# Optimization experiments

Measured on AMD Instinct MI355X. Metric: run time of the kernel, lower is better.

## Reference

```python
import jax, jax.numpy as jnp
import numpy as np

B, D_IN, H, D_OUT = 2048, 1024, 2048, 1024
MAX_STEPS = 12
EPS = 0.01


def setup_inputs() -> dict:
    key = jax.random.key(0)
    ks = jax.random.split(key, 8)
    s_in = 1.0 / np.sqrt(D_IN + H)
    s_h = 1.0 / np.sqrt(H)
    return {
        "x": jax.random.normal(ks[0], (B, D_IN), jnp.float32),
        "h": jax.random.normal(ks[1], (B, H), jnp.float32),
        "W_hidden": jax.random.normal(ks[2], (H, D_IN + H), jnp.float32) * s_in,
        "b_hidden": jnp.zeros((H,), jnp.float32),
        "w_halt": jax.random.normal(ks[3], (H,), jnp.float32) * s_h,
        "b_halt": jnp.float32(-2.0),  # bias low so several ponder steps are taken
        "W_out": jax.random.normal(ks[4], (D_OUT, H), jnp.float32) * s_h,
        "b_out": jnp.zeros((D_OUT,), jnp.float32),
    }


def reference(x, h, W_hidden, b_hidden, w_halt, b_halt, W_out, b_out):
    # Batched ACT halting loop, unrolled to MAX_STEPS via lax.scan.
    def step(s, t):
        # step 0 of the original uses x+1 as a "first step" flag
        xin = jnp.where(t == 0, x + 1.0, x)          # [B, D_IN]
        z = jnp.concatenate([xin, s], axis=-1)        # [B, D_IN+H]
        s_new = z @ W_hidden.T + b_hidden             # [B, H]
        p = jax.nn.sigmoid(s_new @ w_halt + b_halt)   # [B]
        out = s_new @ W_out.T + b_out                 # [B, D_OUT]
        return s_new, (s_new, p, out)

    _, (states, probs, outs) = jax.lax.scan(step, h, jnp.arange(MAX_STEPS))
    # states: [T,B,H], probs: [T,B], outs: [T,B,D_OUT]

    cum = jnp.cumsum(probs, axis=0)                   # [T,B]
    reached = cum >= (1.0 - EPS)
    # first step where cumulative halt prob crosses the threshold (cap at T-1)
    n = jnp.where(jnp.any(reached, axis=0), jnp.argmax(reached, axis=0), MAX_STEPS - 1)  # [B]

    t_idx = jnp.arange(MAX_STEPS)[:, None]            # [T,1]
    before = t_idx < n[None, :]                       # [T,B]
    R = 1.0 - jnp.sum(jnp.where(before, probs, 0.0), axis=0)  # [B] remainder
    w = jnp.where(before, probs, jnp.where(t_idx == n[None, :], R[None, :], 0.0))  # [T,B]

    output = jnp.einsum("tb,tbd->bd", w, outs)        # [B, D_OUT]
    hidden = jnp.einsum("tb,tbh->bh", w, states)      # [B, H]
    ponder = (n + 1).astype(jnp.float32) + R          # [B]
    return output, hidden, ponder
```

## Files before the change

kernel.cpp:

```cpp
#include <hip/hip_runtime.h>
#include <hip/hip_bf16.h>
#include <cstdint>

#define B_SZ   2048
#define D_INN  1024
#define H_SZ   2048
#define D_OUTN 1024
#define TMAX   12
#define LDW    3072
#define NSL    12
#define SLC    256

typedef _Float16 f16;
typedef __attribute__((ext_vector_type(8))) _Float16 f16x8;
typedef __attribute__((ext_vector_type(4))) float    f32x4;

typedef const __attribute__((address_space(1))) uint32_t* gptr_t;
typedef __attribute__((address_space(3))) uint32_t*       lptr_t;
__device__ inline void gld16(const void* g, void* l) {
    __builtin_amdgcn_global_load_lds((gptr_t)g, (lptr_t)l, 16, 0, 0);
}

template<int BN>
__global__ __launch_bounds__(512, 4) void gemm16(
    const f16* __restrict__ A, int lda,
    const f16* __restrict__ Bm, int ldb,
    const f16*  __restrict__ Cadd16,
    const float* __restrict__ radd,
    float* __restrict__ Cf,
    f16* __restrict__ Cs,
    int ldc, int K, int nx)
{
    constexpr int WN = BN / 64;
    constexpr int NV = (BN == 128) ? 3 : 2;
    __shared__ __align__(16) f16 As[3][64 * 64];
    __shared__ __align__(16) f16 Bs[3][BN * 64];
    const int tid  = threadIdx.x;
    const int wave = tid >> 6;
    const int lane = tid & 63;

    const int nwg = gridDim.x;
    const int cpx = nwg >> 3;
    const int bid = (blockIdx.x & 7) * cpx + (blockIdx.x >> 3);
    const int m0 = (bid / nx) * 64, n0 = (bid % nx) * BN;

    const int wr = wave >> 2, wc = wave & 3;
    const int fr = lane & 15, fq = lane >> 4;

    const int acs = tid ^ ((tid >> 3) & 7);
    const f16* gA = A + (size_t)(m0 + (acs >> 3)) * lda + (acs & 7) * 8;
    const int adst = wave << 9;
    const int bcs1 = tid ^ ((tid >> 3) & 7);
    const f16* gB1 = Bm + (size_t)(n0 + (bcs1 >> 3)) * ldb + (bcs1 & 7) * 8;
    const int bdst1 = wave << 9;
    const f16* gB2 = nullptr;
    int bdst2 = 0;
    if constexpr (BN == 128) {
        const int bc2 = tid + 512;
        const int bcs2 = bc2 ^ ((bc2 >> 3) & 7);
        gB2 = Bm + (size_t)(n0 + (bcs2 >> 3)) * ldb + (bcs2 & 7) * 8;
        bdst2 = 4096 + (wave << 9);
    }

    int offA[2][2], offB[WN][2];
#pragma unroll
    for (int m = 0; m < 2; ++m)
#pragma unroll
        for (int ks = 0; ks < 2; ++ks) {
            const int row = wr * 32 + m * 16 + fr;
            offA[m][ks] = row * 64 + (((ks * 4 + fq) ^ (row & 7)) << 3);
        }
#pragma unroll
    for (int n = 0; n < WN; ++n)
#pragma unroll
        for (int ks = 0; ks < 2; ++ks) {
            const int row = wc * (WN * 16) + n * 16 + fr;
            offB[n][ks] = row * 64 + (((ks * 4 + fq) ^ (row & 7)) << 3);
        }

    auto STAGE = [&](int buf, int ko) {
        gld16(gA + ko,  &As[buf][0] + adst);
        gld16(gB1 + ko, &Bs[buf][0] + bdst1);
        if constexpr (BN == 128) gld16(gB2 + ko, &Bs[buf][0] + bdst2);
    };

    f32x4 acc[2][WN] = {};

    STAGE(0, 0);
    const int nk = K >> 6;
    int cur = 0;
    for (int ki = 0; ki < nk; ++ki) {
        const int nxt = (cur == 2) ? 0 : cur + 1;
        if (ki + 1 < nk) {
            STAGE(nxt, (ki + 1) << 6);
            asm volatile("s_waitcnt vmcnt(%0)" :: "i"(NV) : "memory");
        } else {
            asm volatile("s_waitcnt vmcnt(0)" ::: "memory");
        }
        __builtin_amdgcn_s_barrier();
        asm volatile("" ::: "memory");

        f16x8 a[2][2], b[WN][2];
#pragma unroll
        for (int m = 0; m < 2; ++m)
#pragma unroll
            for (int ks = 0; ks < 2; ++ks)
                a[m][ks] = *(const f16x8*)(&As[cur][offA[m][ks]]);
#pragma unroll
        for (int n = 0; n < WN; ++n)
#pragma unroll
            for (int ks = 0; ks < 2; ++ks)
                b[n][ks] = *(const f16x8*)(&Bs[cur][offB[n][ks]]);
#pragma unroll
        for (int ks = 0; ks < 2; ++ks)
#pragma unroll
            for (int m = 0; m < 2; ++m)
#pragma unroll
                for (int n = 0; n < WN; ++n)
                    acc[m][n] = __builtin_amdgcn_mfma_f32_16x16x32_f16(
                        a[m][ks], b[n][ks], acc[m][n], 0, 0, 0);
        cur = nxt;
    }

#pragma unroll
    for (int m = 0; m < 2; ++m) {
#pragma unroll
        for (int n = 0; n < WN; ++n) {
#pragma unroll
            for (int r = 0; r < 4; ++r) {
                const int row = m0 + wr * 32 + m * 16 + fq * 4 + r;
                const int col = n0 + wc * (WN * 16) + n * 16 + fr;
                const size_t o = (size_t)row * ldc + col;
                float v = acc[m][n][r];
                if (Cadd16) v += (float)Cadd16[o];
                if (radd)   v += radd[col];
                if (Cf) Cf[o] = v;
                if (Cs) Cs[o] = (f16)v;
            }
        }
    }
}

__global__ __launch_bounds__(256) void hidacc(
    const f16* __restrict__ s0, const f16* __restrict__ s1,
    const f16* __restrict__ s2, const float* __restrict__ Wmat,
    int tbase, float* __restrict__ hidden, f16* __restrict__ hid16)
{
    const int b = blockIdx.x;
    const float w0 = Wmat[(size_t)(tbase + 0) * B_SZ + b];
    const float w1 = Wmat[(size_t)(tbase + 1) * B_SZ + b];
    const float w2 = Wmat[(size_t)(tbase + 2) * B_SZ + b];
    const bool first = (tbase == 0);
    const bool last  = (tbase == TMAX - 3);
    if (!last && w0 == 0.f && w1 == 0.f && w2 == 0.f) return;

    const int tid = threadIdx.x;
    const size_t o = (size_t)b * H_SZ + tid * 8;
    float hv[8];
    if (first) {
#pragma unroll
        for (int j = 0; j < 8; ++j) hv[j] = 0.f;
    } else {
        const float4 h0 = *(const float4*)(hidden + o);
        const float4 h1 = *(const float4*)(hidden + o + 4);
        hv[0]=h0.x; hv[1]=h0.y; hv[2]=h0.z; hv[3]=h0.w;
        hv[4]=h1.x; hv[5]=h1.y; hv[6]=h1.z; hv[7]=h1.w;
    }
    if (w0 != 0.f) {
        const f16x8 v = *(const f16x8*)(s0 + o);
#pragma unroll
        for (int j = 0; j < 8; ++j) hv[j] += w0 * (float)v[j];
    }
    if (w1 != 0.f) {
        const f16x8 v = *(const f16x8*)(s1 + o);
#pragma unroll
        for (int j = 0; j < 8; ++j) hv[j] += w1 * (float)v[j];
    }
    if (w2 != 0.f) {
        const f16x8 v = *(const f16x8*)(s2 + o);
#pragma unroll
        for (int j = 0; j < 8; ++j) hv[j] += w2 * (float)v[j];
    }
    *(float4*)(hidden + o)     = make_float4(hv[0], hv[1], hv[2], hv[3]);
    *(float4*)(hidden + o + 4) = make_float4(hv[4], hv[5], hv[6], hv[7]);
    if (last) {
        f16x8 hh;
#pragma unroll
        for (int j = 0; j < 8; ++j) hh[j] = (f16)hv[j];
        *(f16x8*)(hid16 + o) = hh;
    }
}

__global__ __launch_bounds__(256) void cast16(
    const float* __restrict__ src, int ld, int cols,
    f16* __restrict__ dst, int total8)
{
    const int i = blockIdx.x * 256 + threadIdx.x;
    if (i >= total8) return;
    const int idx = i * 8;
    const int r = idx / cols, c = idx % cols;
    const float4 v0 = *(const float4*)(src + (size_t)r * ld + c);
    const float4 v1 = *(const float4*)(src + (size_t)r * ld + c + 4);
    f16x8 o;
    o[0]=(f16)v0.x; o[1]=(f16)v0.y; o[2]=(f16)v0.z; o[3]=(f16)v0.w;
    o[4]=(f16)v1.x; o[5]=(f16)v1.y; o[6]=(f16)v1.z; o[7]=(f16)v1.w;
    *(f16x8*)(dst + idx) = o;
}

__global__ __launch_bounds__(256) void rowsum_kernel(
    const float* __restrict__ W, int ld, int K, float* __restrict__ out)
{
    const int j = blockIdx.x;
    const int tid = threadIdx.x;
    float s = 0.f;
    for (int k = tid; k < K; k += 256) s += W[(size_t)j * ld + k];
#pragma unroll
    for (int off = 32; off; off >>= 1) s += __shfl_down(s, off);
    __shared__ float red[4];
    if ((tid & 63) == 0) red[tid >> 6] = s;
    __syncthreads();
    if (tid == 0) out[j] = red[0] + red[1] + red[2] + red[3];
}

__global__ __launch_bounds__(256) void transpose_w(
    const float* __restrict__ in, float* __restrict__ out, int R, int C)
{
    __shared__ float t[32][33];
    const int bc = blockIdx.x * 32, br = blockIdx.y * 32;
    const int tx = threadIdx.x & 31, ty = threadIdx.x >> 5;
#pragma unroll
    for (int i = 0; i < 32; i += 8)
        t[ty + i][tx] = in[(size_t)(br + ty + i) * C + bc + tx];
    __syncthreads();
#pragma unroll
    for (int i = 0; i < 32; i += 8)
        out[(size_t)(bc + ty + i) * R + br + tx] = t[tx][ty + i];
}

__global__ __launch_bounds__(256) void init_u0(
    const float* __restrict__ w, double* __restrict__ u)
{
    const int i = blockIdx.x * 256 + threadIdx.x;
    if (i < H_SZ) u[i] = (double)w[i];
}

__global__ __launch_bounds__(256) void gemv_t(
    const float* __restrict__ WT, const double* __restrict__ uin,
    double* __restrict__ uout)
{
    const int i = blockIdx.x;
    const int tid = threadIdx.x;
    const float* row = WT + (size_t)(D_INN + i) * H_SZ;
    double acc = 0.0;
    for (int j = tid; j < H_SZ; j += 256) acc += (double)row[j] * uin[j];
#pragma unroll
    for (int off = 32; off; off >>= 1) acc += __shfl_down(acc, off);
    __shared__ double red[4];
    if ((tid & 63) == 0) red[tid >> 6] = acc;
    __syncthreads();
    if (tid == 0) uout[i] = red[0] + red[1] + red[2] + red[3];
}

__global__ __launch_bounds__(256) void batch_wx(
    const float* __restrict__ WT, const double* __restrict__ U,
    double* __restrict__ XU, double* __restrict__ XS)
{
    const int k = blockIdx.x;
    const int tid = threadIdx.x;
    const float* row = WT + (size_t)k * H_SZ;
    double au[TMAX] = {}, av[TMAX] = {};
    for (int j = tid; j < H_SZ; j += 256) {
        const double w = (double)row[j];
        double pref = 0.0;
#pragma unroll
        for (int t = 0; t < TMAX; ++t) {
            const double u = U[(size_t)t * H_SZ + j];
            pref += u;
            au[t] += w * u;
            av[t] += w * pref;
        }
    }
    __shared__ double red[4][2 * TMAX];
#pragma unroll
    for (int t = 0; t < TMAX; ++t) {
#pragma unroll
        for (int off = 32; off; off >>= 1) {
            au[t] += __shfl_down(au[t], off);
            av[t] += __shfl_down(av[t], off);
        }
    }
    if ((tid & 63) == 0) {
#pragma unroll
        for (int t = 0; t < TMAX; ++t) {
            red[tid >> 6][t] = au[t];
            red[tid >> 6][TMAX + t] = av[t];
        }
    }
    __syncthreads();
    if (tid == 0) {
#pragma unroll
        for (int t = 0; t < TMAX; ++t) {
            XS[(size_t)t * D_INN + k] = red[0][t] + red[1][t] + red[2][t] + red[3][t];
            XU[(size_t)t * D_INN + k] = red[0][TMAX+t] + red[1][TMAX+t]
                                      + red[2][TMAX+t] + red[3][TMAX+t];
        }
    }
}

__global__ __launch_bounds__(256) void e_kernel(
    const double* __restrict__ XS, const double* __restrict__ U,
    const float* __restrict__ bh, double* __restrict__ E)
{
    const int t = blockIdx.x;
    const int tid = threadIdx.x;
    double a = 0.0;
    for (int k = tid; k < D_INN; k += 256) a += XS[(size_t)t * D_INN + k];
    for (int j = tid; j < H_SZ; j += 256) {
        double v = 0.0;
        for (int s = 0; s <= t; ++s) v += U[(size_t)s * H_SZ + j];
        a += v * (double)bh[j];
    }
#pragma unroll
    for (int off = 32; off; off >>= 1) a += __shfl_down(a, off);
    __shared__ double red[4];
    if ((tid & 63) == 0) red[tid >> 6] = a;
    __syncthreads();
    if (tid == 0) E[t] = red[0] + red[1] + red[2] + red[3];
}

__global__ __launch_bounds__(256) void d_part(
    const float* __restrict__ h, const float* __restrict__ x,
    const double* __restrict__ U, const double* __restrict__ XU,
    double* __restrict__ part)
{
    __shared__ double Us[TMAX][SLC];
    const int blk = blockIdx.x;
    const int sl  = blk % NSL;
    const int br  = (blk / NSL) * 32;
    const int tid = threadIdx.x;
    const int col0 = sl * SLC;
    const bool isH = col0 < H_SZ;
#pragma unroll
    for (int t = 0; t < TMAX; ++t)
        Us[t][tid] = isH ? U[(size_t)(t + 1) * H_SZ + col0 + tid]
                         : XU[(size_t)t * D_INN + (col0 - H_SZ) + tid];
    __syncthreads();
    const int lane8 = tid & 7;
    const int row   = tid >> 3;
    const float* src = isH ? (h + (size_t)(br + row) * H_SZ + col0)
                           : (x + (size_t)(br + row) * D_INN + (col0 - H_SZ));
    double acc[TMAX] = {};
#pragma unroll
    for (int i = 0; i < 8; ++i) {
        const int c = i * 32 + lane8 * 4;
        const float4 v4 = *(const float4*)(src + c);
        const float vv[4] = {v4.x, v4.y, v4.z, v4.w};
#pragma unroll
        for (int j = 0; j < 4; ++j) {
            const double v = (double)vv[j];
#pragma unroll
            for (int t = 0; t < TMAX; ++t) acc[t] += v * Us[t][c + j];
        }
    }
#pragma unroll
    for (int t = 0; t < TMAX; ++t) {
        acc[t] += __shfl_xor(acc[t], 1, 64);
        acc[t] += __shfl_xor(acc[t], 2, 64);
        acc[t] += __shfl_xor(acc[t], 4, 64);
    }
    if (lane8 == 0) {
#pragma unroll
        for (int t = 0; t < TMAX; ++t)
            part[((size_t)(br + row) * NSL + sl) * TMAX + t] = acc[t];
    }
}

__global__ __launch_bounds__(256) void sched_kernel(
    const double* __restrict__ part, const double* __restrict__ E,
    const float* __restrict__ b_halt,
    float* __restrict__ Wmat, float* __restrict__ ponder)
{
    const int b = blockIdx.x * 256 + threadIdx.x;
    if (b >= B_SZ) return;
    const float bh = b_halt[0];
    float cum = 0.f, R = 0.f;
    int n = -1;
    float w[TMAX];
#pragma unroll
    for (int t = 0; t < TMAX; ++t) {
        double dd = E[t];
#pragma unroll
        for (int sl = 0; sl < NSL; ++sl)
            dd += part[((size_t)b * NSL + sl) * TMAX + t];
        const float p = 1.f / (1.f + expf(-((float)dd + bh)));
        if (n < 0) {
            const float c = cum + p;
            if (c >= 0.99f || t == TMAX - 1) { n = t; R = 1.f - cum; w[t] = R; }
            else { w[t] = p; cum = c; }
        } else {
            w[t] = 0.f;
        }
    }
    ponder[b] = (float)(n + 1) + R;
#pragma unroll
    for (int t = 0; t < TMAX; ++t) Wmat[(size_t)t * B_SZ + b] = w[t];
}

extern "C" void kernel_launch(void* const* d_in, const int* in_sizes, int n_in,
                              void* d_out, int out_size, void* d_ws, size_t ws_size,
                              hipStream_t stream)
{
    const float* x        = (const float*)d_in[0];
    const float* h        = (const float*)d_in[1];
    const float* W_hidden = (const float*)d_in[2];
    const float* b_hidden = (const float*)d_in[3];
    const float* w_halt   = (const float*)d_in[4];
    const float* b_halt   = (const float*)d_in[5];
    const float* W_out    = (const float*)d_in[6];
    const float* b_out    = (const float*)d_in[7];

    float* out    = (float*)d_out;
    float* output = out;
    float* hidden = out + (size_t)B_SZ * D_OUTN;
    float* ponder = hidden + (size_t)B_SZ * H_SZ;

    double* U    = (double*)d_ws;
    double* XU   = U  + (size_t)(TMAX + 1) * H_SZ;
    double* XS   = XU + (size_t)TMAX * D_INN;
    double* E    = XS + (size_t)TMAX * D_INN;
    double* part = E + 16;
    float* rsum  = (float*)(part + (size_t)B_SZ * NSL * TMAX);
    float* Wmat  = rsum + H_SZ;
    float* WT    = Wmat + (size_t)TMAX * B_SZ;
    f16* xc16  = (f16*)WT;
    f16* S2    = (f16*)(WT + (size_t)2 * 1024 * 1024);
    f16* hid16 = (f16*)(WT + (size_t)4 * 1024 * 1024);
    f16* xh   = (f16*)(WT + (size_t)LDW * H_SZ);
    f16* Wxh  = xh  + (size_t)B_SZ * D_INN;
    f16* S0   = xh;
    f16* h16  = Wxh + (size_t)H_SZ * D_INN;
    f16* S1   = h16 + (size_t)B_SZ * H_SZ;
    f16* Wsh  = S1  + (size_t)B_SZ * H_SZ;
    f16* Woh  = Wsh + (size_t)H_SZ * H_SZ;

    const dim3 blk(256);
    const dim3 gblk(512);

    cast16<<<dim3(B_SZ * D_INN / 8 / 256), blk, 0, stream>>>(
        x, D_INN, D_INN, xh, B_SZ * D_INN / 8);
    cast16<<<dim3(B_SZ * H_SZ / 8 / 256), blk, 0, stream>>>(
        h, H_SZ, H_SZ, h16, B_SZ * H_SZ / 8);
    cast16<<<dim3(H_SZ * D_INN / 8 / 256), blk, 0, stream>>>(
        W_hidden, LDW, D_INN, Wxh, H_SZ * D_INN / 8);
    cast16<<<dim3(H_SZ * H_SZ / 8 / 256), blk, 0, stream>>>(
        W_hidden + D_INN, LDW, H_SZ, Wsh, H_SZ * H_SZ / 8);
    cast16<<<dim3(D_OUTN * H_SZ / 8 / 256), blk, 0, stream>>>(
        W_out, H_SZ, H_SZ, Woh, D_OUTN * H_SZ / 8);

    rowsum_kernel<<<dim3(H_SZ), blk, 0, stream>>>(W_hidden, LDW, D_INN, rsum);

    transpose_w<<<dim3(LDW / 32, H_SZ / 32), blk, 0, stream>>>(
        W_hidden, WT, H_SZ, LDW);
    init_u0<<<dim3(H_SZ / 256), blk, 0, stream>>>(w_halt, U);
    for (int k = 0; k < TMAX; ++k)
        gemv_t<<<dim3(H_SZ), blk, 0, stream>>>(WT, U + (size_t)k * H_SZ,
                                               U + (size_t)(k + 1) * H_SZ);
    batch_wx<<<dim3(D_INN), blk, 0, stream>>>(WT, U, XU, XS);
    e_kernel<<<dim3(TMAX), blk, 0, stream>>>(XS, U, b_hidden, E);
    d_part<<<dim3((B_SZ / 32) * NSL), blk, 0, stream>>>(h, x, U, XU, part);
    sched_kernel<<<dim3(B_SZ / 256), blk, 0, stream>>>(part, E, b_halt,
                                                       Wmat, ponder);

    gemm16<128><<<dim3((B_SZ / 64) * (H_SZ / 128)), gblk, 0, stream>>>(
        xh, D_INN, Wxh, D_INN, nullptr, b_hidden, nullptr, xc16,
        H_SZ, D_INN, H_SZ / 128);

    f16* Sb[3] = {S0, S1, S2};
    const f16* prev = h16;
    for (int t = 0; t < TMAX; ++t) {
        f16* curS = Sb[t % 3];
        gemm16<128><<<dim3((B_SZ / 64) * (H_SZ / 128)), gblk, 0, stream>>>(
            prev, H_SZ, Wsh, H_SZ, xc16, (t == 0) ? rsum : nullptr,
            nullptr, curS, H_SZ, H_SZ, H_SZ / 128);
        prev = curS;
        if ((t % 3) == 2)
            hidacc<<<dim3(B_SZ), blk, 0, stream>>>(
                S0, S1, S2, Wmat, t - 2, hidden, hid16);
    }

    gemm16<64><<<dim3((B_SZ / 64) * (D_OUTN / 64)), gblk, 0, stream>>>(
        hid16, H_SZ, Woh, H_SZ, nullptr, b_out, output, nullptr,
        D_OUTN, H_SZ, D_OUTN / 64);
}
```

Measured before the change: 551.9 us.

## Fuse cast kernels and replace gemv launch chain with cooperative kernel

Merges the five fp16 cast launches into one kernel that dispatches on block index. It also replaces the init plus twelve sequential gemv_t launches with a single cooperative kernel, which uses grid-wide syncs between steps and has each block handle 8 rows. The goal is to cut launch overhead and the idle gaps between these small kernels. The cost is that the cooperative launch runs only 256 blocks, so each step has less parallelism, and grid.sync adds its own overhead.

```diff
diff --git a/kernel.cpp b/kernel.cpp
--- a/kernel.cpp
+++ b/kernel.cpp
@@ -1,6 +1,9 @@
 #include <hip/hip_runtime.h>
 #include <hip/hip_bf16.h>
+#include <hip/hip_cooperative_groups.h>
 #include <cstdint>
+
+namespace cg = cooperative_groups;
 
 #define B_SZ   2048
 #define D_INN  1024
@@ -191,16 +194,25 @@
     }
 }
 
-__global__ __launch_bounds__(256) void cast16(
-    const float* __restrict__ src, int ld, int cols,
-    f16* __restrict__ dst, int total8)
-{
-    const int i = blockIdx.x * 256 + threadIdx.x;
-    if (i >= total8) return;
-    const int idx = i * 8;
+__global__ __launch_bounds__(256) void cast_all(
+    const float* __restrict__ x, const float* __restrict__ h,
+    const float* __restrict__ Wh, const float* __restrict__ Wo,
+    f16* __restrict__ xh, f16* __restrict__ h16, f16* __restrict__ Wxh,
+    f16* __restrict__ Wsh, f16* __restrict__ Woh)
+{
+    const int b = blockIdx.x;
+    const int tid = threadIdx.x;
+    const float* src; f16* dst; int ld, cols, vidx;
+    if (b < 1024)      { src = x;          dst = xh;  ld = D_INN; cols = D_INN; vidx = b * 256 + tid; }
+    else if (b < 3072) { src = h;          dst = h16; ld = H_SZ;  cols = H_SZ;  vidx = (b - 1024) * 256 + tid; }
+    else if (b < 4096) { src = Wh;         dst = Wxh; ld = LDW;   cols = D_INN; vidx = (b - 3072) * 256 + tid; }
+    else if (b < 6144) { src = Wh + D_INN; dst = Wsh; ld = LDW;   cols = H_SZ;  vidx = (b - 4096) * 256 + tid; }
+    else               { src = Wo;         dst = Woh; ld = H_SZ;  cols = H_SZ;  vidx = (b - 6144) * 256 + tid; }
+    const int idx = vidx * 8;
     const int r = idx / cols, c = idx % cols;
-    const float4 v0 = *(const float4*)(src + (size_t)r * ld + c);
-    const float4 v1 = *(const float4*)(src + (size_t)r * ld + c + 4);
+    const float* p = src + (size_t)r * ld + c;
+    const float4 v0 = *(const float4*)p;
+    const float4 v1 = *(const float4*)(p + 4);
     f16x8 o;
     o[0]=(f16)v0.x; o[1]=(f16)v0.y; o[2]=(f16)v0.z; o[3]=(f16)v0.w;
     o[4]=(f16)v1.x; o[5]=(f16)v1.y; o[6]=(f16)v1.z; o[7]=(f16)v1.w;
@@ -237,28 +249,36 @@
         out[(size_t)(bc + ty + i) * R + br + tx] = t[tx][ty + i];
 }
 
-__global__ __launch_bounds__(256) void init_u0(
-    const float* __restrict__ w, double* __restrict__ u)
-{
-    const int i = blockIdx.x * 256 + threadIdx.x;
-    if (i < H_SZ) u[i] = (double)w[i];
-}
-
-__global__ __launch_bounds__(256) void gemv_t(
-    const float* __restrict__ WT, const double* __restrict__ uin,
-    double* __restrict__ uout)
-{
-    const int i = blockIdx.x;
-    const int tid = threadIdx.x;
-    const float* row = WT + (size_t)(D_INN + i) * H_SZ;
-    double acc = 0.0;
-    for (int j = tid; j < H_SZ; j += 256) acc += (double)row[j] * uin[j];
-#pragma unroll
-    for (int off = 32; off; off >>= 1) acc += __shfl_down(acc, off);
+__global__ __launch_bounds__(256) void u_chain(
+    const float* __restrict__ WT, const float* __restrict__ w_halt,
+    double* __restrict__ U)
+{
+    cg::grid_group grid = cg::this_grid();
+    const int blk = blockIdx.x;
+    const int tid = threadIdx.x;
+    for (int i = blk * 256 + tid; i < H_SZ; i += 256 * 256)
+        U[i] = (double)w_halt[i];
+    grid.sync();
     __shared__ double red[4];
-    if ((tid & 63) == 0) red[tid >> 6] = acc;
-    __syncthreads();
-    if (tid == 0) uout[i] = red[0] + red[1] + red[2] + red[3];
+    for (int k = 0; k < TMAX; ++k) {
+        const double* uin = U + (size_t)k * H_SZ;
+        double* uout = U + (size_t)(k + 1) * H_SZ;
+#pragma unroll
+        for (int r = 0; r < 8; ++r) {
+            const int i = blk * 8 + r;
+            const float* row = WT + (size_t)(D_INN + i) * H_SZ;
+            double acc = 0.0;
+            for (int j = tid; j < H_SZ; j += 256)
+                acc += (double)row[j] * uin[j];
+#pragma unroll
+            for (int off = 32; off; off >>= 1) acc += __shfl_down(acc, off);
+            if ((tid & 63) == 0) red[tid >> 6] = acc;
+            __syncthreads();
+            if (tid == 0) uout[i] = red[0] + red[1] + red[2] + red[3];
+            __syncthreads();
+        }
+        grid.sync();
+    }
 }
 
 __global__ __launch_bounds__(256) void batch_wx(
@@ -446,25 +466,21 @@
     const dim3 blk(256);
     const dim3 gblk(512);
 
-    cast16<<<dim3(B_SZ * D_INN / 8 / 256), blk, 0, stream>>>(
-        x, D_INN, D_INN, xh, B_SZ * D_INN / 8);
-    cast16<<<dim3(B_SZ * H_SZ / 8 / 256), blk, 0, stream>>>(
-        h, H_SZ, H_SZ, h16, B_SZ * H_SZ / 8);
-    cast16<<<dim3(H_SZ * D_INN / 8 / 256), blk, 0, stream>>>(
-        W_hidden, LDW, D_INN, Wxh, H_SZ * D_INN / 8);
-    cast16<<<dim3(H_SZ * H_SZ / 8 / 256), blk, 0, stream>>>(
-        W_hidden + D_INN, LDW, H_SZ, Wsh, H_SZ * H_SZ / 8);
-    cast16<<<dim3(D_OUTN * H_SZ / 8 / 256), blk, 0, stream>>>(
-        W_out, H_SZ, H_SZ, Woh, D_OUTN * H_SZ / 8);
+    cast_all<<<dim3(7168), blk, 0, stream>>>(
+        x, h, W_hidden, W_out, xh, h16, Wxh, Wsh, Woh);
 
     rowsum_kernel<<<dim3(H_SZ), blk, 0, stream>>>(W_hidden, LDW, D_INN, rsum);
 
     transpose_w<<<dim3(LDW / 32, H_SZ / 32), blk, 0, stream>>>(
         W_hidden, WT, H_SZ, LDW);
-    init_u0<<<dim3(H_SZ / 256), blk, 0, stream>>>(w_halt, U);
-    for (int k = 0; k < TMAX; ++k)
-        gemv_t<<<dim3(H_SZ), blk, 0, stream>>>(WT, U + (size_t)k * H_SZ,
-                                               U + (size_t)(k + 1) * H_SZ);
+    {
+        const float* whp = w_halt;
+        const float* wtp = WT;
+        double* up = U;
+        void* args[] = {(void*)&wtp, (void*)&whp, (void*)&up};
+        hipLaunchCooperativeKernel((void*)u_chain, dim3(256), blk, args, 0,
+                                   stream);
+    }
     batch_wx<<<dim3(D_INN), blk, 0, stream>>>(WT, U, XU, XS);
     e_kernel<<<dim3(TMAX), blk, 0, stream>>>(XS, U, b_hidden, E);
     d_part<<<dim3((B_SZ / 32) * NSL), blk, 0, stream>>>(h, x, U, XU, part);
```

After: 978.4 us. 77.3% more time.
